# Optimization experiments

Hardware: AMD Instinct MI355X
Metric: run time of the kernel (lower is better)

The kernel has to match this reference:

```python
import jax, jax.numpy as jnp
import numpy as np

B, L, C = 4, 4096, 1024
NH, CS = 16, 16
HF = C // NH            # 64
NC = L // CS            # 256
LR = 1.0


def setup_inputs() -> dict:
    key = jax.random.key(0)
    ks = jax.random.split(key, 9)
    s = 0.02
    return {
        "hidden_states": jax.random.normal(ks[0], (B, L, C), jnp.float32),
        "Wq": jax.random.normal(ks[1], (C, C), jnp.float32) * s,
        "Wk": jax.random.normal(ks[2], (C, C), jnp.float32) * s,
        "Wv": jax.random.normal(ks[3], (C, C), jnp.float32) * s,
        "Wo": jax.random.normal(ks[4], (C, C), jnp.float32) * s,
        "ilr_w": jax.random.normal(ks[5], (C, NH), jnp.float32) * s,
        "ilr_b": jnp.zeros((NH,), jnp.float32),
        "W1": jax.random.normal(ks[6], (NH, HF, 4 * HF), jnp.float32) * s,
        "W2": jax.random.normal(ks[7], (NH, 4 * HF, HF), jnp.float32) * s,
    }


def _split(x):
    # [B,L,C] -> [B,NH,NC,CS,HF]
    return x.reshape(B, NC, CS, NH, HF).transpose(0, 3, 1, 2, 4)


def reference(hidden_states, Wq, Wk, Wv, Wo, ilr_w, ilr_b, W1, W2):
    XC = _split(hidden_states @ Wq)
    XB = _split(hidden_states @ Wk)
    XA = _split(hidden_states @ Wv)

    # inner-loop learning rate: [B,NH,NC,CS,1]
    ilr = jax.nn.sigmoid(hidden_states.reshape(B, NC, CS, C) @ ilr_w + ilr_b)
    ilr = ilr.transpose(0, 3, 1, 2)[..., None]
    token_idx = 1.0 / jnp.arange(1, CS + 1, dtype=jnp.float32)
    coeff = (LR * token_idx).reshape(1, 1, 1, CS, 1) * ilr / HF

    tril = jnp.tril(jnp.ones((CS, CS), hidden_states.dtype))

    # per-(batch,head) inner states
    W1s = jnp.broadcast_to(W1[None], (B, NH, HF, 4 * HF))
    W2s = jnp.broadcast_to(W2[None], (B, NH, 4 * HF, HF))

    def step(carry, xs):
        W1_s, W2_s = carry
        XA_c, XB_c, XC_c, coeff_c = xs          # [B,NH,CS,HF], coeff [B,NH,CS,1]
        coeff_last = coeff_c[..., -1:, :]        # [B,NH,1,1]
        Z1 = XB_c @ W1_s                         # [B,NH,CS,4HF]
        Z2 = Z1 @ W2_s                           # [B,NH,CS,HF]
        g2 = Z2 - XA_c
        g1 = g2 @ jnp.swapaxes(W2_s, -1, -2)
        Attn1 = tril * (XC_c @ jnp.swapaxes(XB_c, -1, -2))
        Z1_bar = XC_c @ W1_s - coeff_c * (Attn1 @ g1)
        W1_s = W1_s - jnp.swapaxes(coeff_last * XB_c, -1, -2) @ g1
        Attn2 = tril * (Z1_bar @ jnp.swapaxes(Z1, -1, -2))
        Z2_bar = Z1_bar @ W2_s - coeff_c * (Attn2 @ g2)
        W2_s = W2_s - jnp.swapaxes(coeff_last * Z1, -1, -2) @ g2
        return (W1_s, W2_s), Z2_bar

    # move chunk axis to front for scan: [NC,B,NH,CS,*]
    xs = tuple(t.transpose(2, 0, 1, 3, 4) for t in (XA, XB, XC, coeff))
    _, Z2_bars = jax.lax.scan(step, (W1s, W2s), xs)

    # [NC,B,NH,CS,HF] -> [B,NC,CS,NH,HF] -> [B,L,C]
    out = Z2_bars.transpose(1, 0, 3, 2, 4).reshape(B, L, C)
    return out @ Wo
```

## Files before the change

kernel.cpp:

```cpp
#include <hip/hip_runtime.h>

#define Bsz  4
#define Lsz  4096
#define Csz  1024
#define NHsz 16
#define CSsz 16
#define HFsz 64
#define HF4sz 256
#define NCsz 256

typedef __attribute__((ext_vector_type(8))) short  bhalf8;
typedef __attribute__((ext_vector_type(4))) float  floatx4;

__device__ __forceinline__ unsigned short bf_rne(float x) {
  const unsigned u = __float_as_uint(x);
  return (unsigned short)((u + 0x7fffu + ((u >> 16) & 1u)) >> 16);
}
__device__ __forceinline__ void split_rne(float x, unsigned short& h, unsigned short& l) {
  h = bf_rne(x);
  const float hf = __uint_as_float((unsigned)h << 16);
  l = bf_rne(x - hf);
}
__device__ __forceinline__ void tsplit(float x, unsigned short& h, unsigned short& l) {
  const unsigned u = __float_as_uint(x);
  h = (unsigned short)(u >> 16);
  const float r = x - __uint_as_float(u & 0xffff0000u);
  l = bf_rne(r);
}
__device__ __forceinline__ void split_frag8(const float* __restrict__ x,
                                            bhalf8& h, bhalf8& l) {
#pragma unroll
  for (int e = 0; e < 8; ++e) {
    unsigned short hs, ls;
    tsplit(x[e], hs, ls);
    h[e] = (short)hs; l[e] = (short)ls;
  }
}
__device__ __forceinline__ float recon2(unsigned short h, unsigned short l) {
  return __uint_as_float((unsigned)h << 16) + __uint_as_float((unsigned)l << 16);
}

#define MFMA3(acc, ah, al, bh, bl)                                            \
  acc = __builtin_amdgcn_mfma_f32_16x16x32_bf16(ah, bh, acc, 0, 0, 0);        \
  acc = __builtin_amdgcn_mfma_f32_16x16x32_bf16(ah, bl, acc, 0, 0, 0);        \
  acc = __builtin_amdgcn_mfma_f32_16x16x32_bf16(al, bh, acc, 0, 0, 0);

__global__ __launch_bounds__(256)
void split32(const float* __restrict__ in, unsigned short* __restrict__ hi,
             unsigned short* __restrict__ lo)
{
  const int i = (blockIdx.x * 256 + threadIdx.x) * 4;
  const float4 v = *(const float4*)&in[i];
  ushort4 h, l;
  split_rne(v.x, h.x, l.x);
  split_rne(v.y, h.y, l.y);
  split_rne(v.z, h.z, l.z);
  split_rne(v.w, h.w, l.w);
  *(ushort4*)&hi[i] = h;
  *(ushort4*)&lo[i] = l;
}

__global__ __launch_bounds__(256)
void gemm_mfma(const unsigned short* __restrict__ Ahi,
               const unsigned short* __restrict__ Alo,
               const float* __restrict__ Bm,
               float* __restrict__ Cm, int M, int N, int K)
{
  __shared__ unsigned short sAh[128 * 40];
  __shared__ unsigned short sAl[128 * 40];
  __shared__ unsigned short sBh[128 * 40];
  __shared__ unsigned short sBl[128 * 40];

  const int t    = threadIdx.x;
  const int lane = t & 63, w = t >> 6;
  const int wr   = (w >> 1) * 64, wc = (w & 1) * 64;
  const int row0 = blockIdx.y * 128, col0 = blockIdx.x * 128;
  const int fr   = lane & 15, fk = (lane >> 4) * 8;

  floatx4 acc[4][4];
#pragma unroll
  for (int mi = 0; mi < 4; ++mi)
#pragma unroll
    for (int ni = 0; ni < 4; ++ni) acc[mi][ni] = (floatx4){0.f, 0.f, 0.f, 0.f};

  const int arow = t >> 1, akg = (t & 1) * 16;
  const int bc4  = (t & 31) * 4, bk4 = (t >> 5) * 4;

  for (int k0 = 0; k0 < K; k0 += 32) {
    {
      const size_t ga = (size_t)(row0 + arow) * K + k0 + akg;
      const bhalf8 h0 = *(const bhalf8*)&Ahi[ga];
      const bhalf8 h1 = *(const bhalf8*)&Ahi[ga + 8];
      const bhalf8 l0 = *(const bhalf8*)&Alo[ga];
      const bhalf8 l1 = *(const bhalf8*)&Alo[ga + 8];
      *(bhalf8*)&sAh[arow * 40 + akg]     = h0;
      *(bhalf8*)&sAh[arow * 40 + akg + 8] = h1;
      *(bhalf8*)&sAl[arow * 40 + akg]     = l0;
      *(bhalf8*)&sAl[arow * 40 + akg + 8] = l1;
    }
    {
      const float4 r0 = *(const float4*)&Bm[(size_t)(k0 + bk4 + 0) * N + col0 + bc4];
      const float4 r1 = *(const float4*)&Bm[(size_t)(k0 + bk4 + 1) * N + col0 + bc4];
      const float4 r2 = *(const float4*)&Bm[(size_t)(k0 + bk4 + 2) * N + col0 + bc4];
      const float4 r3 = *(const float4*)&Bm[(size_t)(k0 + bk4 + 3) * N + col0 + bc4];
#define STORE_BCOL(v0, v1, v2, v3, c) do {                                   \
      unsigned short h0_, h1_, h2_, h3_, l0_, l1_, l2_, l3_;                 \
      split_rne(v0, h0_, l0_); split_rne(v1, h1_, l1_);                      \
      split_rne(v2, h2_, l2_); split_rne(v3, h3_, l3_);                      \
      const int off_ = (bc4 + (c)) * 40 + bk4;                               \
      *(unsigned*)&sBh[off_]     = (unsigned)h0_ | ((unsigned)h1_ << 16);    \
      *(unsigned*)&sBh[off_ + 2] = (unsigned)h2_ | ((unsigned)h3_ << 16);    \
      *(unsigned*)&sBl[off_]     = (unsigned)l0_ | ((unsigned)l1_ << 16);    \
      *(unsigned*)&sBl[off_ + 2] = (unsigned)l2_ | ((unsigned)l3_ << 16);    \
    } while (0)
      STORE_BCOL(r0.x, r1.x, r2.x, r3.x, 0);
      STORE_BCOL(r0.y, r1.y, r2.y, r3.y, 1);
      STORE_BCOL(r0.z, r1.z, r2.z, r3.z, 2);
      STORE_BCOL(r0.w, r1.w, r2.w, r3.w, 3);
#undef STORE_BCOL
    }
    __syncthreads();

    bhalf8 ah[4], al[4];
#pragma unroll
    for (int mi = 0; mi < 4; ++mi) {
      ah[mi] = *(const bhalf8*)&sAh[(wr + mi * 16 + fr) * 40 + fk];
      al[mi] = *(const bhalf8*)&sAl[(wr + mi * 16 + fr) * 40 + fk];
    }
#pragma unroll
    for (int ni = 0; ni < 4; ++ni) {
      const bhalf8 bh = *(const bhalf8*)&sBh[(wc + ni * 16 + fr) * 40 + fk];
      const bhalf8 bl = *(const bhalf8*)&sBl[(wc + ni * 16 + fr) * 40 + fk];
#pragma unroll
      for (int mi = 0; mi < 4; ++mi) {
        acc[mi][ni] = __builtin_amdgcn_mfma_f32_16x16x32_bf16(ah[mi], bh, acc[mi][ni], 0, 0, 0);
        acc[mi][ni] = __builtin_amdgcn_mfma_f32_16x16x32_bf16(ah[mi], bl, acc[mi][ni], 0, 0, 0);
        acc[mi][ni] = __builtin_amdgcn_mfma_f32_16x16x32_bf16(al[mi], bh, acc[mi][ni], 0, 0, 0);
      }
    }
    __syncthreads();
  }

  const int er = (lane >> 4) * 4;
#pragma unroll
  for (int mi = 0; mi < 4; ++mi)
#pragma unroll
    for (int ni = 0; ni < 4; ++ni) {
      const size_t base = (size_t)(row0 + wr + mi * 16 + er) * N + col0 + wc + ni * 16 + fr;
#pragma unroll
      for (int j = 0; j < 4; ++j)
        Cm[base + (size_t)j * N] = acc[mi][ni][j];
    }
}

__global__ __launch_bounds__(256)
void ilr_coeff(const float* __restrict__ H, const float* __restrict__ Wil,
               const float* __restrict__ bil, float* __restrict__ coeff)
{
  __shared__ float sRow[4][1024];
  __shared__ float sP[4][16][17];
  const int t = threadIdx.x;
  const size_t r0 = (size_t)blockIdx.x * 4;
  for (int rr = 0; rr < 4; ++rr)
    for (int c = t; c < 1024; c += 256)
      sRow[rr][c] = H[(r0 + rr) * 1024 + c];
  __syncthreads();
  const int hh = t & 15, sl = t >> 4;
  for (int rr = 0; rr < 4; ++rr) {
    float acc = 0.f;
    for (int kk = 0; kk < 64; ++kk)
      acc += sRow[rr][sl * 64 + kk] * Wil[(sl * 64 + kk) * 16 + hh];
    sP[rr][sl][hh] = acc;
  }
  __syncthreads();
  if (t < 64) {
    const int rr = t >> 4, h2 = t & 15;
    float s = 0.f;
    for (int sl2 = 0; sl2 < 16; ++sl2) s += sP[rr][sl2][h2];
    s += bil[h2];
    const float sig = 1.f / (1.f + expf(-s));
    const int r  = (int)(r0 + rr);
    const int b  = r >> 12, l = r & 4095, nc = l >> 4, cs = l & 15;
    coeff[((b * 16 + h2) * NCsz + nc) * CSsz + cs] = sig / ((float)(cs + 1) * 64.0f);
  }
}

__global__ __launch_bounds__(512)
void ttt_scan(const float* __restrict__ XA, const float* __restrict__ XBuf,
              const float* __restrict__ XCbuf, const float* __restrict__ coeff,
              const float* __restrict__ W1g, const float* __restrict__ W2g,
              float* __restrict__ Out)
{
  __shared__ __attribute__((aligned(16))) unsigned short sW2h[256 * 72];
  __shared__ __attribute__((aligned(16))) unsigned short sW2l[256 * 72];
  __shared__ __attribute__((aligned(16))) unsigned short sZ1h[16 * 264];
  __shared__ __attribute__((aligned(16))) unsigned short sZ1l[16 * 264];
  __shared__ __attribute__((aligned(16))) unsigned short sZbh[16 * 264];
  __shared__ __attribute__((aligned(16))) unsigned short sZbl[16 * 264];
  __shared__ __attribute__((aligned(16))) float sZ1t[256 * 20];
  __shared__ __attribute__((aligned(16))) float sG1 [256 * 20];
  __shared__ __attribute__((aligned(16))) unsigned short sg2h[16 * 72];
  __shared__ __attribute__((aligned(16))) unsigned short sg2l[16 * 72];
  __shared__ __attribute__((aligned(16))) float sXBt[64 * 20];
  __shared__ __attribute__((aligned(16))) float sA1 [16 * 17];
  __shared__ __attribute__((aligned(16))) float sA2p[4 * 16 * 17];
  __shared__ __attribute__((aligned(16))) float sCo [2 * 16];

  const int t    = threadIdx.x;
  const int bh   = blockIdx.x;
  const int b    = bh >> 4, h = bh & 15;
  const bool isA = (t < 512 / 2);
  const int lane = t & 63;
  const int fr   = lane & 15, fg = lane >> 4;
  const int w    = t >> 6;
  const int tb   = t - 256;
  const int wb   = (t >> 6) & 3;
  const int m    = 16 * wb + fr;

  float w1m[64];
  float w2m[64];
  floatx4 zba[4];
  floatx4 zb2;
  float xar[4];

  const float* W1h = W1g + h * HFsz * HF4sz;
  const float* W2h = W2g + h * HF4sz * HFsz;
  if (isA) {
#pragma unroll
    for (int tt = 0; tt < 4; ++tt)
#pragma unroll
      for (int ks = 0; ks < 2; ++ks)
#pragma unroll
        for (int e = 0; e < 8; ++e)
          w1m[tt * 16 + ks * 8 + e] = W1h[(32 * ks + 8 * fg + e) * 256 + (64 * w + 16 * tt + fr)];
  } else {
#pragma unroll
    for (int ks = 0; ks < 8; ++ks)
#pragma unroll
      for (int e = 0; e < 8; ++e)
        w2m[ks * 8 + e] = W2h[(32 * ks + 8 * fg + e) * 64 + m];
#pragma unroll
    for (int ks = 0; ks < 8; ++ks)
#pragma unroll
      for (int e = 0; e < 8; ++e) {
        const int k = 32 * ks + 8 * fg + e;
        unsigned short hs, ls;
        tsplit(w2m[ks * 8 + e], hs, ls);
        sW2h[k * 72 + m] = hs;
        sW2l[k * 72 + m] = ls;
      }
    const int cb0 = (b * Lsz) * Csz + h * HFsz;
#pragma unroll
    for (int j = 0; j < 4; ++j)
      xar[j] = XA[cb0 + (4 * fg + j) * 1024 + m];
  }
  __syncthreads();

#pragma unroll 1
  for (int nc = 0; nc < NCsz; ++nc) {
    const int cur = nc & 1;
    const int cb  = (b * Lsz + nc * CSsz) * Csz + h * HFsz;
    const int nc1 = (nc + 1) & (NCsz - 1);
    const int cb1 = (b * Lsz + nc1 * CSsz) * Csz + h * HFsz;
    const float* __restrict__ xbG = XBuf  + cb;
    const float* __restrict__ xcG = XCbuf + cb;

    if (isA) {
      if (t < 16) sCo[cur * 16 + t] = coeff[(bh * NCsz + nc) * CSsz + t];
      const float* __restrict__ xbp = xbG + fr * 1024 + 8 * fg;
      const float* __restrict__ xcp = xcG + fr * 1024 + 8 * fg;
      {
        floatx4 acc[4];
#pragma unroll
        for (int tt = 0; tt < 4; ++tt) acc[tt] = (floatx4){0.f, 0.f, 0.f, 0.f};
#pragma unroll
        for (int ks = 0; ks < 2; ++ks) {
          float xv[8];
          *(float4*)&xv[0] = *(const float4*)&xbp[32 * ks];
          *(float4*)&xv[4] = *(const float4*)&xbp[32 * ks + 4];
          bhalf8 xh, xl; split_frag8(xv, xh, xl);
#pragma unroll
          for (int tt = 0; tt < 4; ++tt) {
            bhalf8 wh, wl; split_frag8(&w1m[tt * 16 + ks * 8], wh, wl);
            MFMA3(acc[tt], xh, xl, wh, wl);
          }
        }
#pragma unroll
        for (int tt = 0; tt < 4; ++tt) {
          const int n = 64 * w + 16 * tt + fr;
#pragma unroll
          for (int j = 0; j < 4; ++j) {
            const int i = 4 * fg + j;
            const float v = acc[tt][j];
            unsigned short hs, ls; tsplit(v, hs, ls);
            sZ1h[i * 264 + n] = hs;
            sZ1l[i * 264 + n] = ls;
            sZ1t[n * 20 + i]  = v;
          }
        }
      }
      {
#pragma unroll
        for (int tt = 0; tt < 4; ++tt) zba[tt] = (floatx4){0.f, 0.f, 0.f, 0.f};
#pragma unroll
        for (int ks = 0; ks < 2; ++ks) {
          float xv[8];
          *(float4*)&xv[0] = *(const float4*)&xcp[32 * ks];
          *(float4*)&xv[4] = *(const float4*)&xcp[32 * ks + 4];
          bhalf8 xh, xl; split_frag8(xv, xh, xl);
#pragma unroll
          for (int tt = 0; tt < 4; ++tt) {
            bhalf8 wh, wl; split_frag8(&w1m[tt * 16 + ks * 8], wh, wl);
            MFMA3(zba[tt], xh, xl, wh, wl);
          }
        }
      }
    } else {
      const int ia = tb >> 4, ja = tb & 15;
      float a0 = 0.f, a1 = 0.f;
      if (ja <= ia) {
#pragma unroll
        for (int k = 0; k < 64; k += 8) {
          const float4 c0 = *(const float4*)&xcG[ia * 1024 + k];
          const float4 b0 = *(const float4*)&xbG[ja * 1024 + k];
          const float4 c1 = *(const float4*)&xcG[ia * 1024 + k + 4];
          const float4 b1 = *(const float4*)&xbG[ja * 1024 + k + 4];
          a0 = fmaf(c0.w, b0.w, fmaf(c0.z, b0.z, fmaf(c0.y, b0.y, fmaf(c0.x, b0.x, a0))));
          a1 = fmaf(c1.w, b1.w, fmaf(c1.z, b1.z, fmaf(c1.y, b1.y, fmaf(c1.x, b1.x, a1))));
        }
      }
      sA1[ia * 17 + ja] = a0 + a1;
    }
    __syncthreads();

    if (!isA) {
      floatx4 z2a = (floatx4){0.f, 0.f, 0.f, 0.f};
#pragma unroll
      for (int ks = 0; ks < 8; ++ks) {
        const bhalf8 ah = *(const bhalf8*)&sZ1h[fr * 264 + 32 * ks + 8 * fg];
        const bhalf8 al = *(const bhalf8*)&sZ1l[fr * 264 + 32 * ks + 8 * fg];
        bhalf8 wh, wl; split_frag8(&w2m[ks * 8], wh, wl);
        MFMA3(z2a, ah, al, wh, wl);
      }
#pragma unroll
      for (int j = 0; j < 4; ++j) {
        const int i = 4 * fg + j;
        const float g2v = z2a[j] - xar[j];
        unsigned short hs, ls; tsplit(g2v, hs, ls);
        sg2h[i * 72 + m] = hs;
        sg2l[i * 72 + m] = ls;
      }
    } else {
      const int ir = t >> 4, k4 = (t & 15) * 4;
      const float4 v = *(const float4*)&xbG[ir * 1024 + k4];
      sXBt[(k4 + 0) * 20 + ir] = v.x;
      sXBt[(k4 + 1) * 20 + ir] = v.y;
      sXBt[(k4 + 2) * 20 + ir] = v.z;
      sXBt[(k4 + 3) * 20 + ir] = v.w;
    }
    __syncthreads();

    if (!isA) {
      floatx4 g1a[4];
#pragma unroll
      for (int r = 0; r < 4; ++r) g1a[r] = (floatx4){0.f, 0.f, 0.f, 0.f};
#pragma unroll
      for (int ks2 = 0; ks2 < 2; ++ks2) {
        const bhalf8 gh = *(const bhalf8*)&sg2h[fr * 72 + 32 * ks2 + 8 * fg];
        const bhalf8 gl = *(const bhalf8*)&sg2l[fr * 72 + 32 * ks2 + 8 * fg];
#pragma unroll
        for (int r = 0; r < 4; ++r) {
          const int rt = 4 * wb + r;
          const bhalf8 ah = *(const bhalf8*)&sW2h[(16 * rt + fr) * 72 + 32 * ks2 + 8 * fg];
          const bhalf8 al = *(const bhalf8*)&sW2l[(16 * rt + fr) * 72 + 32 * ks2 + 8 * fg];
          MFMA3(g1a[r], ah, al, gh, gl);
        }
      }
#pragma unroll
      for (int r = 0; r < 4; ++r) {
        const int rt = 4 * wb + r;
#pragma unroll
        for (int j = 0; j < 4; ++j)
          sG1[(16 * rt + 4 * fg + j) * 20 + fr] = g1a[r][j];
      }
    }
    __syncthreads();

    if (isA) {
#pragma unroll
      for (int tt = 0; tt < 4; ++tt) {
        const int n = 64 * w + 16 * tt + fr;
        float gv[16];
        *(float4*)&gv[0]  = *(const float4*)&sG1[n * 20 + 0];
        *(float4*)&gv[4]  = *(const float4*)&sG1[n * 20 + 4];
        *(float4*)&gv[8]  = *(const float4*)&sG1[n * 20 + 8];
        *(float4*)&gv[12] = *(const float4*)&sG1[n * 20 + 12];
#pragma unroll
        for (int j = 0; j < 4; ++j) {
          const int i = 4 * fg + j;
          float at = 0.f;
#pragma unroll
          for (int jp = 0; jp < 16; ++jp)
            at = fmaf(sA1[i * 17 + jp], gv[jp], at);
          const float z = zba[tt][j] - sCo[cur * 16 + i] * at;
          unsigned short hs, ls; tsplit(z, hs, ls);
          sZbh[i * 264 + n] = hs;
          sZbl[i * 264 + n] = ls;
        }
      }
    }
    __syncthreads();

    if (isA) {
      floatx4 a2 = (floatx4){0.f, 0.f, 0.f, 0.f};
#pragma unroll
      for (int ksl = 0; ksl < 2; ++ksl) {
        const int ks = 2 * w + ksl;
        const bhalf8 ah = *(const bhalf8*)&sZbh[fr * 264 + 32 * ks + 8 * fg];
        const bhalf8 al = *(const bhalf8*)&sZbl[fr * 264 + 32 * ks + 8 * fg];
        const bhalf8 bhf = *(const bhalf8*)&sZ1h[fr * 264 + 32 * ks + 8 * fg];
        const bhalf8 blf = *(const bhalf8*)&sZ1l[fr * 264 + 32 * ks + 8 * fg];
        MFMA3(a2, ah, al, bhf, blf);
      }
#pragma unroll
      for (int j = 0; j < 4; ++j) {
        const int i = 4 * fg + j;
        sA2p[w * 272 + i * 17 + fr] = (fr <= i) ? a2[j] : 0.f;
      }
      const float cl = sCo[cur * 16 + 15];
#pragma unroll
      for (int i = 0; i < 16; ++i) {
        float cg[4];
#pragma unroll
        for (int tt = 0; tt < 4; ++tt)
          cg[tt] = cl * sG1[(64 * w + 16 * tt + fr) * 20 + i];
#pragma unroll
        for (int ks = 0; ks < 2; ++ks)
#pragma unroll
          for (int e = 0; e < 8; ++e) {
            const float xb = sXBt[(32 * ks + 8 * fg + e) * 20 + i];
#pragma unroll
            for (int tt = 0; tt < 4; ++tt)
              w1m[tt * 16 + ks * 8 + e] = fmaf(-cg[tt], xb, w1m[tt * 16 + ks * 8 + e]);
          }
      }
    } else {
      zb2 = (floatx4){0.f, 0.f, 0.f, 0.f};
#pragma unroll
      for (int ks = 0; ks < 8; ++ks) {
        const bhalf8 ah = *(const bhalf8*)&sZbh[fr * 264 + 32 * ks + 8 * fg];
        const bhalf8 al = *(const bhalf8*)&sZbl[fr * 264 + 32 * ks + 8 * fg];
        bhalf8 wh, wl; split_frag8(&w2m[ks * 8], wh, wl);
        MFMA3(zb2, ah, al, wh, wl);
      }
      const float cl = sCo[cur * 16 + 15];
      float cg[16];
#pragma unroll
      for (int i = 0; i < 16; ++i)
        cg[i] = cl * recon2(sg2h[i * 72 + m], sg2l[i * 72 + m]);
#pragma unroll
      for (int ks = 0; ks < 8; ++ks)
#pragma unroll
        for (int e = 0; e < 8; ++e) {
          const int k = 32 * ks + 8 * fg + e;
          float zr[16];
          *(float4*)&zr[0]  = *(const float4*)&sZ1t[k * 20 + 0];
          *(float4*)&zr[4]  = *(const float4*)&sZ1t[k * 20 + 4];
          *(float4*)&zr[8]  = *(const float4*)&sZ1t[k * 20 + 8];
          *(float4*)&zr[12] = *(const float4*)&sZ1t[k * 20 + 12];
          float acc = w2m[ks * 8 + e];
#pragma unroll
          for (int i = 0; i < 16; ++i) acc = fmaf(-cg[i], zr[i], acc);
          w2m[ks * 8 + e] = acc;
        }
    }
    __syncthreads();

    if (!isA) {
      float at[4] = {0.f, 0.f, 0.f, 0.f};
#pragma unroll
      for (int jp = 0; jp < 16; ++jp) {
        const float g2v = recon2(sg2h[jp * 72 + m], sg2l[jp * 72 + m]);
#pragma unroll
        for (int j = 0; j < 4; ++j) {
          const int i = 4 * fg + j;
          const float a2s = sA2p[i * 17 + jp] + sA2p[272 + i * 17 + jp]
                          + sA2p[544 + i * 17 + jp] + sA2p[816 + i * 17 + jp];
          at[j] = fmaf(a2s, g2v, at[j]);
        }
      }
#pragma unroll
      for (int j = 0; j < 4; ++j) {
        const int i = 4 * fg + j;
        Out[cb + i * 1024 + m] = zb2[j] - sCo[cur * 16 + i] * at[j];
      }
#pragma unroll
      for (int ks = 0; ks < 8; ++ks)
#pragma unroll
        for (int e = 0; e < 8; ++e) {
          const int k = 32 * ks + 8 * fg + e;
          unsigned short hs, ls;
          tsplit(w2m[ks * 8 + e], hs, ls);
          sW2h[k * 72 + m] = hs;
          sW2l[k * 72 + m] = ls;
        }
#pragma unroll
      for (int j = 0; j < 4; ++j)
        xar[j] = XA[cb1 + (4 * fg + j) * 1024 + m];
    }
  }
}

extern "C" void kernel_launch(void* const* d_in, const int* in_sizes, int n_in,
                              void* d_out, int out_size, void* d_ws, size_t ws_size,
                              hipStream_t stream)
{
  const float* H    = (const float*)d_in[0];
  const float* Wq   = (const float*)d_in[1];
  const float* Wk   = (const float*)d_in[2];
  const float* Wv   = (const float*)d_in[3];
  const float* Wo   = (const float*)d_in[4];
  const float* Wil  = (const float*)d_in[5];
  const float* bil  = (const float*)d_in[6];
  const float* W1   = (const float*)d_in[7];
  const float* W2   = (const float*)d_in[8];
  float* out        = (float*)d_out;

  float* ws    = (float*)d_ws;
  float* bXC   = ws;
  float* bXB   = ws + 16777216;
  float* bZ2b  = ws + 33554432;
  float* bCo   = ws + 50331648;
  float* bXA   = out;

  unsigned short* hHi = (unsigned short*)bZ2b;
  unsigned short* hLo = hHi + 16777216;
  unsigned short* zHi = (unsigned short*)bXC;
  unsigned short* zLo = zHi + 16777216;

  const int M = Bsz * Lsz, N = Csz, K = Csz;
  dim3 gm(N / 128, M / 128);
  dim3 bm(256);

  split32<<<16384, 256, 0, stream>>>(H, hHi, hLo);
  gemm_mfma<<<gm, bm, 0, stream>>>(hHi, hLo, Wq, bXC, M, N, K);
  gemm_mfma<<<gm, bm, 0, stream>>>(hHi, hLo, Wk, bXB, M, N, K);
  gemm_mfma<<<gm, bm, 0, stream>>>(hHi, hLo, Wv, bXA, M, N, K);
  ilr_coeff<<<M / 4, 256, 0, stream>>>(H, Wil, bil, bCo);
  ttt_scan<<<Bsz * NHsz, 512, 0, stream>>>(bXA, bXB, bXC, bCo, W1, W2, bZ2b);
  split32<<<16384, 256, 0, stream>>>(bZ2b, zHi, zLo);
  gemm_mfma<<<gm, bm, 0, stream>>>(zHi, zLo, Wo, out, M, N, K);
}
```

Before: 8.694 ms.

## Rebalance TTT scan phases and swizzle shared-memory layouts to cut bank conflicts

Moves the XC@W1 product from the first phase of the A-warp group into the phase where the B group computes g1, which balances work between the two thread halves across barriers. W2 in shared memory moves to an XOR-swizzled 64-wide layout, XB is stored row-major, and Z1t float4 writes and reads are rotated, all to reduce LDS bank conflicts and replace scalar transposed stores. The XA prefetch for the next chunk is issued earlier, and the W2 rank-update loop is split in halves to lower register pressure. The risk is more index arithmetic and a chance of swizzle mismatches between the writes and reads.

Measured after the change: 11.23 ms. +29.1%, slower.

```diff
diff --git a/kernel.cpp b/kernel.cpp
--- a/kernel.cpp
+++ b/kernel.cpp
@@ -44,6 +44,8 @@
   acc = __builtin_amdgcn_mfma_f32_16x16x32_bf16(ah, bh, acc, 0, 0, 0);        \
   acc = __builtin_amdgcn_mfma_f32_16x16x32_bf16(ah, bl, acc, 0, 0, 0);        \
   acc = __builtin_amdgcn_mfma_f32_16x16x32_bf16(al, bh, acc, 0, 0, 0);
+
+#define W2IDX(k, mm) ((k) * 64 + (((((mm) >> 3) ^ ((k) >> 3) ^ (k)) & 7) << 3) + ((mm) & 7))
 
 __global__ __launch_bounds__(256)
 void split32(const float* __restrict__ in, unsigned short* __restrict__ hi,
@@ -191,8 +193,8 @@
               const float* __restrict__ W1g, const float* __restrict__ W2g,
               float* __restrict__ Out)
 {
-  __shared__ __attribute__((aligned(16))) unsigned short sW2h[256 * 72];
-  __shared__ __attribute__((aligned(16))) unsigned short sW2l[256 * 72];
+  __shared__ __attribute__((aligned(16))) unsigned short sW2h[256 * 64];
+  __shared__ __attribute__((aligned(16))) unsigned short sW2l[256 * 64];
   __shared__ __attribute__((aligned(16))) unsigned short sZ1h[16 * 264];
   __shared__ __attribute__((aligned(16))) unsigned short sZ1l[16 * 264];
   __shared__ __attribute__((aligned(16))) unsigned short sZbh[16 * 264];
@@ -201,7 +203,7 @@
   __shared__ __attribute__((aligned(16))) float sG1 [256 * 20];
   __shared__ __attribute__((aligned(16))) unsigned short sg2h[16 * 72];
   __shared__ __attribute__((aligned(16))) unsigned short sg2l[16 * 72];
-  __shared__ __attribute__((aligned(16))) float sXBt[64 * 20];
+  __shared__ __attribute__((aligned(16))) float sXBt[16 * 68];
   __shared__ __attribute__((aligned(16))) float sA1 [16 * 17];
   __shared__ __attribute__((aligned(16))) float sA2p[4 * 16 * 17];
   __shared__ __attribute__((aligned(16))) float sCo [2 * 16];
@@ -209,7 +211,7 @@
   const int t    = threadIdx.x;
   const int bh   = blockIdx.x;
   const int b    = bh >> 4, h = bh & 15;
-  const bool isA = (t < 512 / 2);
+  const bool isA = (t < 256);
   const int lane = t & 63;
   const int fr   = lane & 15, fg = lane >> 4;
   const int w    = t >> 6;
@@ -246,8 +248,9 @@
         const int k = 32 * ks + 8 * fg + e;
         unsigned short hs, ls;
         tsplit(w2m[ks * 8 + e], hs, ls);
-        sW2h[k * 72 + m] = hs;
-        sW2l[k * 72 + m] = ls;
+        const int idx = W2IDX(k, m);
+        sW2h[idx] = hs;
+        sW2l[idx] = ls;
       }
     const int cb0 = (b * Lsz) * Csz + h * HFsz;
 #pragma unroll
@@ -268,52 +271,32 @@
     if (isA) {
       if (t < 16) sCo[cur * 16 + t] = coeff[(bh * NCsz + nc) * CSsz + t];
       const float* __restrict__ xbp = xbG + fr * 1024 + 8 * fg;
-      const float* __restrict__ xcp = xcG + fr * 1024 + 8 * fg;
-      {
-        floatx4 acc[4];
-#pragma unroll
-        for (int tt = 0; tt < 4; ++tt) acc[tt] = (floatx4){0.f, 0.f, 0.f, 0.f};
-#pragma unroll
-        for (int ks = 0; ks < 2; ++ks) {
-          float xv[8];
-          *(float4*)&xv[0] = *(const float4*)&xbp[32 * ks];
-          *(float4*)&xv[4] = *(const float4*)&xbp[32 * ks + 4];
-          bhalf8 xh, xl; split_frag8(xv, xh, xl);
-#pragma unroll
-          for (int tt = 0; tt < 4; ++tt) {
-            bhalf8 wh, wl; split_frag8(&w1m[tt * 16 + ks * 8], wh, wl);
-            MFMA3(acc[tt], xh, xl, wh, wl);
-          }
-        }
-#pragma unroll
-        for (int tt = 0; tt < 4; ++tt) {
-          const int n = 64 * w + 16 * tt + fr;
-#pragma unroll
-          for (int j = 0; j < 4; ++j) {
-            const int i = 4 * fg + j;
-            const float v = acc[tt][j];
-            unsigned short hs, ls; tsplit(v, hs, ls);
-            sZ1h[i * 264 + n] = hs;
-            sZ1l[i * 264 + n] = ls;
-            sZ1t[n * 20 + i]  = v;
-          }
-        }
-      }
-      {
-#pragma unroll
-        for (int tt = 0; tt < 4; ++tt) zba[tt] = (floatx4){0.f, 0.f, 0.f, 0.f};
-#pragma unroll
-        for (int ks = 0; ks < 2; ++ks) {
-          float xv[8];
-          *(float4*)&xv[0] = *(const float4*)&xcp[32 * ks];
-          *(float4*)&xv[4] = *(const float4*)&xcp[32 * ks + 4];
-          bhalf8 xh, xl; split_frag8(xv, xh, xl);
-#pragma unroll
-          for (int tt = 0; tt < 4; ++tt) {
-            bhalf8 wh, wl; split_frag8(&w1m[tt * 16 + ks * 8], wh, wl);
-            MFMA3(zba[tt], xh, xl, wh, wl);
-          }
-        }
+      float xv[8];
+      bhalf8 xh0, xl0, xh1, xl1;
+      *(float4*)&xv[0] = *(const float4*)&xbp[0];
+      *(float4*)&xv[4] = *(const float4*)&xbp[4];
+      split_frag8(xv, xh0, xl0);
+      *(float4*)&xv[0] = *(const float4*)&xbp[32];
+      *(float4*)&xv[4] = *(const float4*)&xbp[36];
+      split_frag8(xv, xh1, xl1);
+#pragma unroll
+      for (int tt = 0; tt < 4; ++tt) {
+        bhalf8 wh, wl;
+        floatx4 acc = (floatx4){0.f, 0.f, 0.f, 0.f};
+        split_frag8(&w1m[tt * 16], wh, wl);
+        MFMA3(acc, xh0, xl0, wh, wl);
+        split_frag8(&w1m[tt * 16 + 8], wh, wl);
+        MFMA3(acc, xh1, xl1, wh, wl);
+        const int n = 64 * w + 16 * tt + fr;
+#pragma unroll
+        for (int j = 0; j < 4; ++j) {
+          const int i = 4 * fg + j;
+          unsigned short hs, ls; tsplit(acc[j], hs, ls);
+          sZ1h[i * 264 + n] = hs;
+          sZ1l[i * 264 + n] = ls;
+        }
+        const int rotn = (n >> 3) & 3;
+        *(float4*)&sZ1t[n * 20 + ((fg ^ rotn) << 2)] = *(float4*)&acc;
       }
     } else {
       const int ia = tb >> 4, ja = tb & 15;
@@ -352,36 +335,55 @@
       }
     } else {
       const int ir = t >> 4, k4 = (t & 15) * 4;
-      const float4 v = *(const float4*)&xbG[ir * 1024 + k4];
-      sXBt[(k4 + 0) * 20 + ir] = v.x;
-      sXBt[(k4 + 1) * 20 + ir] = v.y;
-      sXBt[(k4 + 2) * 20 + ir] = v.z;
-      sXBt[(k4 + 3) * 20 + ir] = v.w;
+      *(float4*)&sXBt[ir * 68 + k4] = *(const float4*)&xbG[ir * 1024 + k4];
     }
     __syncthreads();
 
     if (!isA) {
-      floatx4 g1a[4];
-#pragma unroll
-      for (int r = 0; r < 4; ++r) g1a[r] = (floatx4){0.f, 0.f, 0.f, 0.f};
-#pragma unroll
-      for (int ks2 = 0; ks2 < 2; ++ks2) {
-        const bhalf8 gh = *(const bhalf8*)&sg2h[fr * 72 + 32 * ks2 + 8 * fg];
-        const bhalf8 gl = *(const bhalf8*)&sg2l[fr * 72 + 32 * ks2 + 8 * fg];
-#pragma unroll
-        for (int r = 0; r < 4; ++r) {
-          const int rt = 4 * wb + r;
-          const bhalf8 ah = *(const bhalf8*)&sW2h[(16 * rt + fr) * 72 + 32 * ks2 + 8 * fg];
-          const bhalf8 al = *(const bhalf8*)&sW2l[(16 * rt + fr) * 72 + 32 * ks2 + 8 * fg];
-          MFMA3(g1a[r], ah, al, gh, gl);
-        }
-      }
+      const bhalf8 gh0 = *(const bhalf8*)&sg2h[fr * 72 + 8 * fg];
+      const bhalf8 gl0 = *(const bhalf8*)&sg2l[fr * 72 + 8 * fg];
+      const bhalf8 gh1 = *(const bhalf8*)&sg2h[fr * 72 + 32 + 8 * fg];
+      const bhalf8 gl1 = *(const bhalf8*)&sg2l[fr * 72 + 32 + 8 * fg];
 #pragma unroll
       for (int r = 0; r < 4; ++r) {
-        const int rt = 4 * wb + r;
+        const int rt  = 4 * wb + r;
+        const int row = 16 * rt + fr;
+        const int swzr = ((row >> 3) ^ row) & 7;
+        floatx4 acc = (floatx4){0.f, 0.f, 0.f, 0.f};
+        {
+          const int pb = fg ^ swzr;
+          const bhalf8 ah = *(const bhalf8*)&sW2h[row * 64 + (pb << 3)];
+          const bhalf8 al = *(const bhalf8*)&sW2l[row * 64 + (pb << 3)];
+          MFMA3(acc, ah, al, gh0, gl0);
+        }
+        {
+          const int pb = (4 + fg) ^ swzr;
+          const bhalf8 ah = *(const bhalf8*)&sW2h[row * 64 + (pb << 3)];
+          const bhalf8 al = *(const bhalf8*)&sW2l[row * 64 + (pb << 3)];
+          MFMA3(acc, ah, al, gh1, gl1);
+        }
 #pragma unroll
         for (int j = 0; j < 4; ++j)
-          sG1[(16 * rt + 4 * fg + j) * 20 + fr] = g1a[r][j];
+          sG1[(16 * rt + 4 * fg + j) * 20 + fr] = acc[j];
+      }
+    } else {
+      const float* __restrict__ xcp = xcG + fr * 1024 + 8 * fg;
+      float xv[8];
+      bhalf8 xh0, xl0, xh1, xl1;
+      *(float4*)&xv[0] = *(const float4*)&xcp[0];
+      *(float4*)&xv[4] = *(const float4*)&xcp[4];
+      split_frag8(xv, xh0, xl0);
+      *(float4*)&xv[0] = *(const float4*)&xcp[32];
+      *(float4*)&xv[4] = *(const float4*)&xcp[36];
+      split_frag8(xv, xh1, xl1);
+#pragma unroll
+      for (int tt = 0; tt < 4; ++tt) {
+        bhalf8 wh, wl;
+        zba[tt] = (floatx4){0.f, 0.f, 0.f, 0.f};
+        split_frag8(&w1m[tt * 16], wh, wl);
+        MFMA3(zba[tt], xh0, xl0, wh, wl);
+        split_frag8(&w1m[tt * 16 + 8], wh, wl);
+        MFMA3(zba[tt], xh1, xl1, wh, wl);
       }
     }
     __syncthreads();
@@ -408,6 +410,10 @@
           sZbl[i * 264 + n] = ls;
         }
       }
+    } else {
+#pragma unroll
+      for (int j = 0; j < 4; ++j)
+        xar[j] = XA[cb1 + (4 * fg + j) * 1024 + m];
     }
     __syncthreads();
 
@@ -416,8 +422,8 @@
 #pragma unroll
       for (int ksl = 0; ksl < 2; ++ksl) {
         const int ks = 2 * w + ksl;
-        const bhalf8 ah = *(const bhalf8*)&sZbh[fr * 264 + 32 * ks + 8 * fg];
-        const bhalf8 al = *(const bhalf8*)&sZbl[fr * 264 + 32 * ks + 8 * fg];
+        const bhalf8 ah  = *(const bhalf8*)&sZbh[fr * 264 + 32 * ks + 8 * fg];
+        const bhalf8 al  = *(const bhalf8*)&sZbl[fr * 264 + 32 * ks + 8 * fg];
         const bhalf8 bhf = *(const bhalf8*)&sZ1h[fr * 264 + 32 * ks + 8 * fg];
         const bhalf8 blf = *(const bhalf8*)&sZ1l[fr * 264 + 32 * ks + 8 * fg];
         MFMA3(a2, ah, al, bhf, blf);
@@ -430,18 +436,19 @@
       const float cl = sCo[cur * 16 + 15];
 #pragma unroll
       for (int i = 0; i < 16; ++i) {
-        float cg[4];
-#pragma unroll
-        for (int tt = 0; tt < 4; ++tt)
-          cg[tt] = cl * sG1[(64 * w + 16 * tt + fr) * 20 + i];
+        const float cg0 = cl * sG1[(64 * w +  0 + fr) * 20 + i];
+        const float cg1 = cl * sG1[(64 * w + 16 + fr) * 20 + i];
+        const float cg2 = cl * sG1[(64 * w + 32 + fr) * 20 + i];
+        const float cg3 = cl * sG1[(64 * w + 48 + fr) * 20 + i];
 #pragma unroll
         for (int ks = 0; ks < 2; ++ks)
 #pragma unroll
           for (int e = 0; e < 8; ++e) {
-            const float xb = sXBt[(32 * ks + 8 * fg + e) * 20 + i];
-#pragma unroll
-            for (int tt = 0; tt < 4; ++tt)
-              w1m[tt * 16 + ks * 8 + e] = fmaf(-cg[tt], xb, w1m[tt * 16 + ks * 8 + e]);
+            const float xb = sXBt[i * 68 + 32 * ks + 8 * fg + e];
+            w1m[ 0 + ks * 8 + e] = fmaf(-cg0, xb, w1m[ 0 + ks * 8 + e]);
+            w1m[16 + ks * 8 + e] = fmaf(-cg1, xb, w1m[16 + ks * 8 + e]);
+            w1m[32 + ks * 8 + e] = fmaf(-cg2, xb, w1m[32 + ks * 8 + e]);
+            w1m[48 + ks * 8 + e] = fmaf(-cg3, xb, w1m[48 + ks * 8 + e]);
           }
       }
     } else {
@@ -454,25 +461,28 @@
         MFMA3(zb2, ah, al, wh, wl);
       }
       const float cl = sCo[cur * 16 + 15];
-      float cg[16];
-#pragma unroll
-      for (int i = 0; i < 16; ++i)
-        cg[i] = cl * recon2(sg2h[i * 72 + m], sg2l[i * 72 + m]);
-#pragma unroll
-      for (int ks = 0; ks < 8; ++ks)
-#pragma unroll
-        for (int e = 0; e < 8; ++e) {
-          const int k = 32 * ks + 8 * fg + e;
-          float zr[16];
-          *(float4*)&zr[0]  = *(const float4*)&sZ1t[k * 20 + 0];
-          *(float4*)&zr[4]  = *(const float4*)&sZ1t[k * 20 + 4];
-          *(float4*)&zr[8]  = *(const float4*)&sZ1t[k * 20 + 8];
-          *(float4*)&zr[12] = *(const float4*)&sZ1t[k * 20 + 12];
-          float acc = w2m[ks * 8 + e];
-#pragma unroll
-          for (int i = 0; i < 16; ++i) acc = fmaf(-cg[i], zr[i], acc);
-          w2m[ks * 8 + e] = acc;
-        }
+#pragma unroll
+      for (int half = 0; half < 2; ++half) {
+        float cg[8];
+#pragma unroll
+        for (int ii = 0; ii < 8; ++ii)
+          cg[ii] = cl * recon2(sg2h[(half * 8 + ii) * 72 + m],
+                               sg2l[(half * 8 + ii) * 72 + m]);
+#pragma unroll
+        for (int ks = 0; ks < 8; ++ks)
+#pragma unroll
+          for (int e = 0; e < 8; ++e) {
+            const int k = 32 * ks + 8 * fg + e;
+            const float4 z0 = *(const float4*)&sZ1t[k * 20 + (((2 * half + 0) ^ fg) << 2)];
+            const float4 z1 = *(const float4*)&sZ1t[k * 20 + (((2 * half + 1) ^ fg) << 2)];
+            float acc = w2m[ks * 8 + e];
+            acc = fmaf(-cg[0], z0.x, acc); acc = fmaf(-cg[1], z0.y, acc);
+            acc = fmaf(-cg[2], z0.z, acc); acc = fmaf(-cg[3], z0.w, acc);
+            acc = fmaf(-cg[4], z1.x, acc); acc = fmaf(-cg[5], z1.y, acc);
+            acc = fmaf(-cg[6], z1.z, acc); acc = fmaf(-cg[7], z1.w, acc);
+            w2m[ks * 8 + e] = acc;
+          }
+      }
     }
     __syncthreads();
 
@@ -501,12 +511,10 @@
           const int k = 32 * ks + 8 * fg + e;
           unsigned short hs, ls;
           tsplit(w2m[ks * 8 + e], hs, ls);
-          sW2h[k * 72 + m] = hs;
-          sW2l[k * 72 + m] = ls;
-        }
-#pragma unroll
-      for (int j = 0; j < 4; ++j)
-        xar[j] = XA[cb1 + (4 * fg + j) * 1024 + m];
+          const int idx = W2IDX(k, m);
+          sW2h[idx] = hs;
+          sW2l[idx] = ls;
+        }
     }
   }
 }
```
